# Performance work log

Hardware: AMD Instinct MI355X
Metric: run time of the kernel (lower is better)

The kernel has to match this reference:

```python
import jax, jax.numpy as jnp
import numpy as np

B, L, D, N_HEADS = 4, 8192, 1024, 16
HD = D // N_HEADS
MASK_NEG = -1e10


def setup_inputs() -> dict:
    key = jax.random.key(0)
    ks = jax.random.split(key, 5)
    # xavier_normal std for square Dense: sqrt(2/(fan_in+fan_out))
    std = (2.0 / (D + D)) ** 0.5
    return {
        "query": jax.random.normal(ks[0], (B, L, D), dtype=jnp.float32),
        "mask": jax.random.bernoulli(ks[1], 0.1, (B, L)),  # True = masked out
        "Wq": std * jax.random.normal(ks[2], (D, D), dtype=jnp.float32),
        "bq": jnp.zeros((D,), dtype=jnp.float32),
        "Wk": std * jax.random.normal(ks[3], (D, D), dtype=jnp.float32),
        "bk": jnp.zeros((D,), dtype=jnp.float32),
        "Wv": std * jax.random.normal(ks[4], (D, D), dtype=jnp.float32),
        "bv": jnp.zeros((D,), dtype=jnp.float32),
    }


def reference(query, mask, Wq, bq, Wk, bk, Wv, bv):
    # Self-attention: key = value = query (original falls back when key/value are None)
    q = query @ Wq + bq  # [B, L, D]
    k = query @ Wk + bk
    v = query @ Wv + bv
    # split heads: b l (n h) -> b l n h
    qs = q.reshape(B, L, N_HEADS, HD)
    ks_ = k.reshape(B, L, N_HEADS, HD)
    vs = v.reshape(B, L, N_HEADS, HD)
    m = mask[:, :, None, None]  # [B, L, 1, 1], broadcast over heads & dims
    K = jnp.where(m, MASK_NEG, ks_)
    V = jnp.where(m, 0.0, vs)
    # elu kernel feature map: phi(x) = elu(x) + 1 (elu(-1e10)+1 -> 0 for masked keys)
    phiK = jax.nn.elu(K) + 1.0
    phiQ = jax.nn.elu(qs) + 1.0
    # per-head kv summary: [B, N, HD_k, HD_v]
    kv = jnp.einsum('blnk,blnv->bnkv', phiK, V)
    # FAITHFUL to original einsum 'blk,bkv->blk': sums kv over v, elementwise with phiQ
    kv_sum = kv.sum(-1)  # [B, N, HD]
    out = phiQ * kv_sum[:, None, :, :]  # [B, L, N, HD]
    # combine heads: b l n h -> b l (n h)
    return out.reshape(B, L, D)
```

## Files before the change

### kernel.cpp

```cpp
#include <hip/hip_runtime.h>

typedef unsigned short u16;
typedef unsigned int u32;
typedef __attribute__((ext_vector_type(8))) short s16x8;
typedef __attribute__((ext_vector_type(4))) float f32x4;

#define GAS __attribute__((address_space(1)))
#define LAS __attribute__((address_space(3)))

#define BB 4
#define LL 8192
#define DD 1024
#define NH 16
#define HD 64
#define MROWS (BB * LL)
#define NWBT 2176

__device__ __forceinline__ u16 f2bf(float f) {
  u32 u = __builtin_bit_cast(u32, f);
  u32 r = (u + 0x7FFFu + ((u >> 16) & 1u)) >> 16;
  return (u16)r;
}
__device__ __forceinline__ float bf2f(u32 lo) {
  return __builtin_bit_cast(float, lo << 16);
}

__device__ __forceinline__ void async16(const void* g, void* l) {
  __builtin_amdgcn_global_load_lds((const GAS u32*)g, (LAS u32*)l, 16, 0, 0);
}

__device__ __forceinline__ bool get_mask(const void* mp, int row, int mode) {
  if (mode == 2) return ((const unsigned char*)mp)[row] != 0;
  if (mode == 1) return ((const float*)mp)[row] != 0.f;
  return ((const int*)mp)[row] != 0;
}

__global__ void detect_mask(const u32* __restrict__ m, int* __restrict__ flag) {
  int i = blockIdx.x * 256 + threadIdx.x;
  u32 v = m[i];
  int f = 0;
  if (v == 0x3F800000u) f = 1;
  else if (v > 1u) f = 2;
  if (f) atomicMax(flag, f);
}

__global__ void cvt_q(const float* __restrict__ q, u16* __restrict__ qb, int n4) {
  int i = blockIdx.x * 256 + threadIdx.x;
  if (i >= n4) return;
  float4 v = ((const float4*)q)[i];
  u16 o0 = f2bf(v.x), o1 = f2bf(v.y), o2 = f2bf(v.z), o3 = f2bf(v.w);
  ((u32*)qb)[2 * i] = (u32)o0 | ((u32)o1 << 16);
  ((u32*)qb)[2 * i + 1] = (u32)o2 | ((u32)o3 << 16);
}

__global__ void build_wbt(const float* __restrict__ Wq, const float* __restrict__ Wk,
                          u16* __restrict__ WbT) {
  __shared__ float t[32][33];
  const int n0 = blockIdx.x * 32;
  const int k0 = blockIdx.y * 32;
  const float* W = (n0 >> 10) == 0 ? Wq : Wk;
  const int nloc = n0 & 1023;
  const int tx = threadIdx.x, ty = threadIdx.y;
#pragma unroll
  for (int j = 0; j < 32; j += 8)
    t[ty + j][tx] = W[(size_t)(k0 + ty + j) * DD + nloc + tx];
  __syncthreads();
#pragma unroll
  for (int j = 0; j < 32; j += 8)
    WbT[(size_t)(n0 + ty + j) * DD + k0 + tx] = f2bf(t[tx][ty + j]);
}

__global__ void build_wvs(const float* __restrict__ Wv, u16* __restrict__ WbT) {
  int i = blockIdx.x * 256 + threadIdx.x;
  int k = i >> 4, h = i & 15;
  float s = 0.f;
  const float* p = Wv + (size_t)k * DD + h * HD;
#pragma unroll 8
  for (int j = 0; j < 64; ++j) s += p[j];
  WbT[(size_t)(2048 + h) * DD + k] = f2bf(s);
}

__global__ void build_bcat(const float* __restrict__ bq, const float* __restrict__ bk,
                           const float* __restrict__ bv, float* __restrict__ bcat) {
  int i = blockIdx.x * 256 + threadIdx.x;
  if (i < 1024) bcat[i] = bq[i];
  else if (i < 2048) bcat[i] = bk[i - 1024];
  else if (i < 2064) {
    float s = 0.f;
    const float* p = bv + (i - 2048) * HD;
#pragma unroll 8
    for (int j = 0; j < 64; ++j) s += p[j];
    bcat[i] = s;
  } else if (i < NWBT) bcat[i] = 0.f;
}

__global__ __launch_bounds__(256) void gemm_qkv(
    const u16* __restrict__ qb, const u16* __restrict__ WbT,
    const float* __restrict__ bcat, const void* __restrict__ maskp,
    const int* __restrict__ mmode,
    u16* __restrict__ phiQ, float* __restrict__ sV, float* __restrict__ kv,
    int phase) {
  __shared__ u16 ldsA[128 * 64];
  __shared__ u16 ldsB[128 * 64];
  const int tid = threadIdx.x;
  const int lane = tid & 63;
  const int w = tid >> 6;
  const int wm = w & 1, wn = w >> 1;
  const int row0 = blockIdx.x * 128;
  const int cy = blockIdx.y;
  const int col0 = phase == 0 ? (cy == 8 ? 2048 : cy * 128) : 1024 + cy * 128;

  f32x4 acc[4][4] = {};

  const int r_l = tid >> 3;
  const int slot = tid & 7;
  const int seg = slot ^ (r_l & 7);
  const u16* gA = qb + (size_t)(row0 + r_l) * DD + seg * 8;
  const u16* gB = WbT + (size_t)(col0 + r_l) * DD + seg * 8;

  for (int k0 = 0; k0 < DD; k0 += 64) {
    __syncthreads();
#pragma unroll
    for (int i = 0; i < 4; ++i) {
      async16(gA + (size_t)i * 32 * DD + k0, ldsA + (i * 256 + tid) * 8);
      async16(gB + (size_t)i * 32 * DD + k0, ldsB + (i * 256 + tid) * 8);
    }
    __syncthreads();
#pragma unroll
    for (int kk = 0; kk < 2; ++kk) {
      s16x8 af[4], bfr[4];
      const int segk = kk * 4 + (lane >> 4);
#pragma unroll
      for (int mi = 0; mi < 4; ++mi) {
        const int r = wm * 64 + mi * 16 + (lane & 15);
        af[mi] = *(const s16x8*)(ldsA + r * 64 + (segk ^ (r & 7)) * 8);
      }
#pragma unroll
      for (int ni = 0; ni < 4; ++ni) {
        const int r = wn * 64 + ni * 16 + (lane & 15);
        bfr[ni] = *(const s16x8*)(ldsB + r * 64 + (segk ^ (r & 7)) * 8);
      }
#pragma unroll
      for (int mi = 0; mi < 4; ++mi)
#pragma unroll
        for (int ni = 0; ni < 4; ++ni)
          acc[mi][ni] = __builtin_amdgcn_mfma_f32_16x16x32_bf16(af[mi], bfr[ni], acc[mi][ni], 0, 0, 0);
    }
  }

  const int mode = *mmode;
  const int lanec = lane & 15, laneq = lane >> 4;
  const int wcol0 = col0 + wn * 64;

  if (phase == 1) {
    const int n = (wcol0 - 1024) >> 6;
    const int b = row0 >> 13;
    float pc[4] = {0.f, 0.f, 0.f, 0.f};
#pragma unroll
    for (int mi = 0; mi < 4; ++mi) {
#pragma unroll
      for (int r = 0; r < 4; ++r) {
        const int row = row0 + wm * 64 + mi * 16 + laneq * 4 + r;
        const bool msk = get_mask(maskp, row, mode);
        if (!msk) {
          const float sv = sV[(size_t)row * NH + n];
#pragma unroll
          for (int ni = 0; ni < 4; ++ni) {
            const int col = wcol0 + ni * 16 + lanec;
            float v = acc[mi][ni][r] + bcat[col];
            float phi = v > 0.f ? v + 1.f : __expf(v);
            pc[ni] += phi * sv;
          }
        }
      }
    }
#pragma unroll
    for (int ni = 0; ni < 4; ++ni) {
      pc[ni] += __shfl_xor(pc[ni], 16);
      pc[ni] += __shfl_xor(pc[ni], 32);
    }
    if (laneq == 0) {
#pragma unroll
      for (int ni = 0; ni < 4; ++ni) {
        const int colk = wcol0 - 1024 + ni * 16 + lanec;
        atomicAdd(&kv[b * DD + colk], pc[ni]);
      }
    }
  } else if (wcol0 < 2048) {
#pragma unroll
    for (int mi = 0; mi < 4; ++mi) {
#pragma unroll
      for (int r = 0; r < 4; ++r) {
        const int row = row0 + wm * 64 + mi * 16 + laneq * 4 + r;
#pragma unroll
        for (int ni = 0; ni < 4; ++ni) {
          const int col = wcol0 + ni * 16 + lanec;
          float v = acc[mi][ni][r] + bcat[col];
          float phi = v > 0.f ? v + 1.f : __expf(v);
          phiQ[(size_t)row * DD + col] = f2bf(phi);
        }
      }
    }
  } else {
    if (wn == 0) {
#pragma unroll
      for (int mi = 0; mi < 4; ++mi) {
#pragma unroll
        for (int r = 0; r < 4; ++r) {
          const int row = row0 + wm * 64 + mi * 16 + laneq * 4 + r;
          const bool msk = get_mask(maskp, row, mode);
          float v = acc[mi][0][r] + bcat[2048 + lanec];
          if (msk) v = 0.f;
          sV[(size_t)row * NH + lanec] = v;
        }
      }
    }
  }
}

__global__ void finalize(const u16* __restrict__ phiQ, const float* __restrict__ kv_sum,
                         float* __restrict__ out) {
  const size_t i = (size_t)(blockIdx.x * 256 + threadIdx.x) * 4;
  const size_t b = i >> 23;
  const int d = (int)(i & 1023);
  u32 p0 = *(const u32*)(phiQ + i);
  u32 p1 = *(const u32*)(phiQ + i + 2);
  float4 kv = *(const float4*)(kv_sum + b * DD + d);
  float4 o;
  o.x = bf2f(p0 & 0xffffu) * kv.x;
  o.y = bf2f(p0 >> 16) * kv.y;
  o.z = bf2f(p1 & 0xffffu) * kv.z;
  o.w = bf2f(p1 >> 16) * kv.w;
  *(float4*)(out + i) = o;
}

extern "C" void kernel_launch(void* const* d_in, const int* in_sizes, int n_in,
                              void* d_out, int out_size, void* d_ws, size_t ws_size,
                              hipStream_t stream) {
  const float* query = (const float*)d_in[0];
  const void* maskp = d_in[1];
  const float* Wq = (const float*)d_in[2];
  const float* bq = (const float*)d_in[3];
  const float* Wk = (const float*)d_in[4];
  const float* bk = (const float*)d_in[5];
  const float* Wv = (const float*)d_in[6];
  const float* bv = (const float*)d_in[7];
  float* out = (float*)d_out;

  char* ws = (char*)d_ws;
  u16* qb = (u16*)ws;            ws += (size_t)MROWS * DD * 2;
  u16* WbT = (u16*)ws;           ws += (size_t)NWBT * DD * 2;
  u16* phiQ = (u16*)ws;          ws += (size_t)MROWS * DD * 2;
  float* sV = (float*)ws;        ws += (size_t)MROWS * NH * 4;
  float* bcat = (float*)ws;      ws += (size_t)NWBT * 4;
  float* kv = (float*)ws;        ws += (size_t)BB * DD * 4;
  int* mflag = (int*)ws;         ws += 256;

  hipMemsetAsync(kv, 0, (size_t)BB * DD * 4 + 256, stream);
  hipMemsetAsync(WbT + (size_t)2064 * DD, 0, (size_t)112 * DD * 2, stream);

  detect_mask<<<32, 256, 0, stream>>>((const u32*)maskp, mflag);
  cvt_q<<<(MROWS * (DD / 4) + 255) / 256, 256, 0, stream>>>(query, qb, MROWS * (DD / 4));
  build_wbt<<<dim3(2048 / 32, DD / 32), dim3(32, 8), 0, stream>>>(Wq, Wk, WbT);
  build_wvs<<<64, 256, 0, stream>>>(Wv, WbT);
  build_bcat<<<(NWBT + 255) / 256, 256, 0, stream>>>(bq, bk, bv, bcat);
  gemm_qkv<<<dim3(MROWS / 128, 9), 256, 0, stream>>>(
      qb, WbT, bcat, maskp, mflag, phiQ, sV, kv, 0);
  gemm_qkv<<<dim3(MROWS / 128, 8), 256, 0, stream>>>(
      qb, WbT, bcat, maskp, mflag, phiQ, sV, kv, 1);
  finalize<<<(MROWS * DD / 4) / 256, 256, 0, stream>>>(phiQ, kv, out);
}
```

Baseline: 485.5 us.

## Fuse query conversion with V-sum projection and fold finalize into Q GEMM epilogue

A new prep_q kernel converts query to bf16 while computing the 16-column summed-V projection via MFMA, replacing the separate conversion kernel and the ninth column tile of the first GEMM. The K-phase GEMM now runs first, so the Q-phase GEMM can multiply phi(Q) by the finished kv sums and write the fp32 output directly. This removes the bf16 phiQ intermediate, its write and re-read, and the finalize kernel. The trade-offs are the fp32 output stores moving into the GEMM epilogue and prep_q doing little MFMA work per loaded tile.

```diff
diff --git a/kernel.cpp b/kernel.cpp
--- a/kernel.cpp
+++ b/kernel.cpp
@@ -14,7 +14,7 @@
 #define NH 16
 #define HD 64
 #define MROWS (BB * LL)
-#define NWBT 2176
+#define NWBT 2064
 
 __device__ __forceinline__ u16 f2bf(float f) {
   u32 u = __builtin_bit_cast(u32, f);
@@ -42,15 +42,6 @@
   if (v == 0x3F800000u) f = 1;
   else if (v > 1u) f = 2;
   if (f) atomicMax(flag, f);
-}
-
-__global__ void cvt_q(const float* __restrict__ q, u16* __restrict__ qb, int n4) {
-  int i = blockIdx.x * 256 + threadIdx.x;
-  if (i >= n4) return;
-  float4 v = ((const float4*)q)[i];
-  u16 o0 = f2bf(v.x), o1 = f2bf(v.y), o2 = f2bf(v.z), o3 = f2bf(v.w);
-  ((u32*)qb)[2 * i] = (u32)o0 | ((u32)o1 << 16);
-  ((u32*)qb)[2 * i + 1] = (u32)o2 | ((u32)o3 << 16);
 }
 
 __global__ void build_wbt(const float* __restrict__ Wq, const float* __restrict__ Wk,
@@ -91,15 +82,88 @@
 #pragma unroll 8
     for (int j = 0; j < 64; ++j) s += p[j];
     bcat[i] = s;
-  } else if (i < NWBT) bcat[i] = 0.f;
+  }
+}
+
+__global__ __launch_bounds__(256) void prep_q(
+    const float* __restrict__ query, const u16* __restrict__ WbT,
+    const float* __restrict__ bcat, const void* __restrict__ maskp,
+    const int* __restrict__ mmode,
+    u16* __restrict__ qb, float* __restrict__ sV) {
+  __shared__ u16 ldsW[16 * 1024];
+  __shared__ u16 ldsA[128 * 64];
+  const int tid = threadIdx.x;
+  const int lane = tid & 63;
+  const int w = tid >> 6;
+  const int row0 = blockIdx.x * 128;
+
+  {
+    const int h = tid & 15;
+    const int cb = tid >> 4;
+#pragma unroll
+    for (int j = 0; j < 8; ++j) {
+      const int c = cb * 8 + j;
+      s16x8 v = *(const s16x8*)(WbT + (size_t)(2048 + h) * DD + c * 8);
+      *(s16x8*)(ldsW + h * 1024 + (c ^ (h & 7)) * 8) = v;
+    }
+  }
+
+  const int r_l = tid >> 3;
+  const int slot = tid & 7;
+  f32x4 acc[2] = {};
+
+  for (int k0 = 0; k0 < DD; k0 += 64) {
+    __syncthreads();
+#pragma unroll
+    for (int i = 0; i < 4; ++i) {
+      const int rl = i * 32 + r_l;
+      const int seg = slot ^ (rl & 7);
+      const float* gp = query + (size_t)(row0 + rl) * DD + k0 + seg * 8;
+      float4 v0 = *(const float4*)gp;
+      float4 v1 = *(const float4*)(gp + 4);
+      s16x8 o;
+      o[0] = (short)f2bf(v0.x); o[1] = (short)f2bf(v0.y);
+      o[2] = (short)f2bf(v0.z); o[3] = (short)f2bf(v0.w);
+      o[4] = (short)f2bf(v1.x); o[5] = (short)f2bf(v1.y);
+      o[6] = (short)f2bf(v1.z); o[7] = (short)f2bf(v1.w);
+      *(s16x8*)(qb + (size_t)(row0 + rl) * DD + k0 + seg * 8) = o;
+      *(s16x8*)(ldsA + rl * 64 + slot * 8) = o;
+    }
+    __syncthreads();
+#pragma unroll
+    for (int kk = 0; kk < 2; ++kk) {
+      const int segk = kk * 4 + (lane >> 4);
+      const int hh = lane & 15;
+      const int cc = (k0 >> 3) + segk;
+      s16x8 bfr = *(const s16x8*)(ldsW + hh * 1024 + (cc ^ (hh & 7)) * 8);
+#pragma unroll
+      for (int mi = 0; mi < 2; ++mi) {
+        const int r = w * 32 + mi * 16 + hh;
+        s16x8 af = *(const s16x8*)(ldsA + r * 64 + ((segk ^ (r & 7))) * 8);
+        acc[mi] = __builtin_amdgcn_mfma_f32_16x16x32_bf16(af, bfr, acc[mi], 0, 0, 0);
+      }
+    }
+  }
+
+  const int mode = *mmode;
+  const int lanec = lane & 15, laneq = lane >> 4;
+#pragma unroll
+  for (int mi = 0; mi < 2; ++mi)
+#pragma unroll
+    for (int r = 0; r < 4; ++r) {
+      const int row = row0 + w * 32 + mi * 16 + laneq * 4 + r;
+      const bool msk = get_mask(maskp, row, mode);
+      float v = acc[mi][r] + bcat[2048 + lanec];
+      sV[(size_t)row * NH + lanec] = msk ? 0.f : v;
+    }
 }
 
 __global__ __launch_bounds__(256) void gemm_qkv(
     const u16* __restrict__ qb, const u16* __restrict__ WbT,
     const float* __restrict__ bcat, const void* __restrict__ maskp,
     const int* __restrict__ mmode,
-    u16* __restrict__ phiQ, float* __restrict__ sV, float* __restrict__ kv,
-    int phase) {
+    const float* __restrict__ sV, float* __restrict__ kv,
+    float* __restrict__ out, int phase) {
   __shared__ u16 ldsA[128 * 64];
   __shared__ u16 ldsB[128 * 64];
   const int tid = threadIdx.x;
@@ -108,7 +172,7 @@
   const int wm = w & 1, wn = w >> 1;
   const int row0 = blockIdx.x * 128;
   const int cy = blockIdx.y;
-  const int col0 = phase == 0 ? (cy == 8 ? 2048 : cy * 128) : 1024 + cy * 128;
+  const int col0 = phase == 0 ? cy * 128 : 1024 + cy * 128;
 
   f32x4 acc[4][4] = {};
 
@@ -151,10 +215,10 @@
   const int mode = *mmode;
   const int lanec = lane & 15, laneq = lane >> 4;
   const int wcol0 = col0 + wn * 64;
+  const int b = row0 >> 13;
 
   if (phase == 1) {
     const int n = (wcol0 - 1024) >> 6;
-    const int b = row0 >> 13;
     float pc[4] = {0.f, 0.f, 0.f, 0.f};
 #pragma unroll
     for (int mi = 0; mi < 4; ++mi) {
@@ -186,7 +250,11 @@
         atomicAdd(&kv[b * DD + colk], pc[ni]);
       }
     }
-  } else if (wcol0 < 2048) {
+  } else {
+    float kvv[4];
+#pragma unroll
+    for (int ni = 0; ni < 4; ++ni)
+      kvv[ni] = kv[b * DD + wcol0 + ni * 16 + lanec];
 #pragma unroll
     for (int mi = 0; mi < 4; ++mi) {
 #pragma unroll
@@ -197,41 +265,11 @@
           const int col = wcol0 + ni * 16 + lanec;
           float v = acc[mi][ni][r] + bcat[col];
           float phi = v > 0.f ? v + 1.f : __expf(v);
-          phiQ[(size_t)row * DD + col] = f2bf(phi);
+          out[(size_t)row * DD + col] = phi * kvv[ni];
         }
       }
     }
-  } else {
-    if (wn == 0) {
-#pragma unroll
-      for (int mi = 0; mi < 4; ++mi) {
-#pragma unroll
-        for (int r = 0; r < 4; ++r) {
-          const int row = row0 + wm * 64 + mi * 16 + laneq * 4 + r;
-          const bool msk = get_mask(maskp, row, mode);
-          float v = acc[mi][0][r] + bcat[2048 + lanec];
-          if (msk) v = 0.f;
-          sV[(size_t)row * NH + lanec] = v;
-        }
-      }
-    }
-  }
-}
-
-__global__ void finalize(const u16* __restrict__ phiQ, const float* __restrict__ kv_sum,
-                         float* __restrict__ out) {
-  const size_t i = (size_t)(blockIdx.x * 256 + threadIdx.x) * 4;
-  const size_t b = i >> 23;
-  const int d = (int)(i & 1023);
-  u32 p0 = *(const u32*)(phiQ + i);
-  u32 p1 = *(const u32*)(phiQ + i + 2);
-  float4 kv = *(const float4*)(kv_sum + b * DD + d);
-  float4 o;
-  o.x = bf2f(p0 & 0xffffu) * kv.x;
-  o.y = bf2f(p0 >> 16) * kv.y;
-  o.z = bf2f(p1 & 0xffffu) * kv.z;
-  o.w = bf2f(p1 >> 16) * kv.w;
-  *(float4*)(out + i) = o;
+  }
 }
 
 extern "C" void kernel_launch(void* const* d_in, const int* in_sizes, int n_in,
@@ -250,23 +288,20 @@
   char* ws = (char*)d_ws;
   u16* qb = (u16*)ws;            ws += (size_t)MROWS * DD * 2;
   u16* WbT = (u16*)ws;           ws += (size_t)NWBT * DD * 2;
-  u16* phiQ = (u16*)ws;          ws += (size_t)MROWS * DD * 2;
   float* sV = (float*)ws;        ws += (size_t)MROWS * NH * 4;
   float* bcat = (float*)ws;      ws += (size_t)NWBT * 4;
   float* kv = (float*)ws;        ws += (size_t)BB * DD * 4;
   int* mflag = (int*)ws;         ws += 256;
 
   hipMemsetAsync(kv, 0, (size_t)BB * DD * 4 + 256, stream);
-  hipMemsetAsync(WbT + (size_t)2064 * DD, 0, (size_t)112 * DD * 2, stream);
 
   detect_mask<<<32, 256, 0, stream>>>((const u32*)maskp, mflag);
-  cvt_q<<<(MROWS * (DD / 4) + 255) / 256, 256, 0, stream>>>(query, qb, MROWS * (DD / 4));
   build_wbt<<<dim3(2048 / 32, DD / 32), dim3(32, 8), 0, stream>>>(Wq, Wk, WbT);
   build_wvs<<<64, 256, 0, stream>>>(Wv, WbT);
   build_bcat<<<(NWBT + 255) / 256, 256, 0, stream>>>(bq, bk, bv, bcat);
-  gemm_qkv<<<dim3(MROWS / 128, 9), 256, 0, stream>>>(
-      qb, WbT, bcat, maskp, mflag, phiQ, sV, kv, 0);
+  prep_q<<<MROWS / 128, 256, 0, stream>>>(query, WbT, bcat, maskp, mflag, qb, sV);
   gemm_qkv<<<dim3(MROWS / 128, 8), 256, 0, stream>>>(
-      qb, WbT, bcat, maskp, mflag, phiQ, sV, kv, 1);
-  finalize<<<(MROWS * DD / 4) / 256, 256, 0, stream>>>(phiQ, kv, out);
-}
+      qb, WbT, bcat, maskp, mflag, sV, kv, out, 1);
+  gemm_qkv<<<dim3(MROWS / 128, 8), 256, 0, stream>>>(
+      qb, WbT, bcat, maskp, mflag, sV, kv, out, 0);
+}
```

Result: faster. 471.8 us (-2.8%).
